# Kernel tuning notes

Measured on AMD Instinct MI355X. Metric: run time of the kernel, lower is better.

The kernel has to match this reference:

```python
import jax, jax.numpy as jnp
import numpy as np

B, L, H = 64, 512, 1024


def _gen_masks():
    rng = np.random.default_rng(0)

    def gen_cat(items_lo, items_hi, w_lo, w_hi, s_lo, s_hi):
        items_per_ex = rng.integers(items_lo, items_hi + 1, size=B)
        word_counts, sub_counts = [], []
        ex_sub = np.zeros(B, np.int64)
        ex_word = np.zeros(B, np.int64)
        for i in range(B):
            for _ in range(int(items_per_ex[i])):
                nw = int(rng.integers(w_lo, w_hi + 1))
                word_counts.append(nw)
                ex_word[i] += nw
                for _ in range(nw):
                    ns = int(rng.integers(s_lo, s_hi + 1))
                    sub_counts.append(ns)
                    ex_sub[i] += ns
        return items_per_ex, np.array(word_counts), np.array(sub_counts), ex_sub, ex_word

    q = gen_cat(1, 1, 8, 15, 1, 3)     # one question per example
    t = gen_cat(3, 6, 1, 3, 1, 3)      # tables per example
    c = gen_cat(12, 25, 1, 4, 1, 3)    # columns per example

    def plm_mask(starts, lens):
        m = np.zeros((B, L), bool)
        for i in range(B):
            m[i, starts[i]:starts[i] + lens[i]] = True
        return m

    qs = np.ones(B, np.int64)
    ts = qs + q[3]
    cs = ts + t[3]
    assert int((cs + c[3]).max()) <= L

    def sub_mask(sc):
        return np.arange(sc.max())[None, :] < sc[:, None]

    masks = dict(
        question_mask_plm=plm_mask(qs, q[3]),
        table_mask_plm=plm_mask(ts, t[3]),
        column_mask_plm=plm_mask(cs, c[3]),
        question_subword_mask=sub_mask(q[2]),
        table_subword_mask=sub_mask(t[2]),
        column_subword_mask=sub_mask(c[2]),
        question_mask=np.arange(q[4].max())[None, :] < q[4][:, None],
        table_word_mask=np.arange(t[1].max())[None, :] < t[1][:, None],
        column_word_mask=np.arange(c[1].max())[None, :] < c[1][:, None],
    )
    return {k: jnp.asarray(v) for k, v in masks.items()}


def setup_inputs() -> dict:
    key = jax.random.key(0)
    k1, k2 = jax.random.split(key)
    inp = _gen_masks()
    inp["inputs"] = jax.random.normal(k1, (B, L, H), jnp.float32)
    inp["W"] = jax.random.normal(k2, (H, H), jnp.float32) * 0.02
    inp["b"] = jnp.zeros((H,), jnp.float32)
    return inp


def _move(values, src_mask, dst_mask):
    """masked_select(src_mask) followed by masked_scatter_(dst_mask):
    the k-th True of src_mask feeds the k-th True of dst_mask (row-major)."""
    Hd = values.shape[-1]
    v = values.reshape(-1, Hd)
    sm = src_mask.reshape(-1)
    n = v.shape[0]
    rank = jnp.cumsum(sm) - 1                       # rank among True positions
    buf = jnp.zeros((n, Hd), v.dtype).at[jnp.where(sm, rank, n)].set(v, mode="drop")
    dm = dst_mask.reshape(-1)
    drank = jnp.clip(jnp.cumsum(dm) - 1, 0, n - 1)
    out = jnp.where(dm[:, None], buf[drank], 0.0)
    return out.reshape(dst_mask.shape + (Hd,))


def _scatter_rows(rows, dst_mask):
    """masked_scatter_ of consecutive row vectors into True slots of dst_mask."""
    dm = dst_mask.reshape(-1)
    rank = jnp.clip(jnp.cumsum(dm) - 1, 0, rows.shape[0] - 1)
    out = jnp.where(dm[:, None], rows[rank], 0.0)
    return out.reshape(dst_mask.shape + (rows.shape[-1],))


def _pool(x, mask, W, b):
    # PoolingFunction(method='mean-pooling'): masked mean over subwords, then Linear+Tanh
    mf = mask.astype(x.dtype)[..., None]
    mean = (x * mf).sum(1) / mf.sum(1)
    return jnp.tanh(mean @ W.T + b)


def _forward(inputs, W, b, m):
    q = _pool(_move(inputs, m["question_mask_plm"], m["question_subword_mask"]),
              m["question_subword_mask"], W, b)
    t = _pool(_move(inputs, m["table_mask_plm"], m["table_subword_mask"]),
              m["table_subword_mask"], W, b)
    c = _pool(_move(inputs, m["column_mask_plm"], m["column_subword_mask"]),
              m["column_subword_mask"], W, b)
    return (_scatter_rows(q, m["question_mask"]),
            _scatter_rows(t, m["table_word_mask"]),
            _scatter_rows(c, m["column_word_mask"]))


def reference(inputs, W, b, question_mask_plm, table_mask_plm, column_mask_plm,
              question_subword_mask, table_subword_mask, column_subword_mask,
              question_mask, table_word_mask, column_word_mask):
    m = dict(question_mask_plm=question_mask_plm, table_mask_plm=table_mask_plm,
             column_mask_plm=column_mask_plm, question_subword_mask=question_subword_mask,
             table_subword_mask=table_subword_mask, column_subword_mask=column_subword_mask,
             question_mask=question_mask, table_word_mask=table_word_mask,
             column_word_mask=column_word_mask)
    return _forward(inputs, W, b, m)
```

## Files before the change

### kernel.cpp

```cpp
#include <hip/hip_runtime.h>
#include <hip/hip_bf16.h>
#include <stdint.h>

#define BB 64
#define LL 512
#define HH 1024

using short8 = __attribute__((ext_vector_type(8))) short;
using f32x4  = __attribute__((ext_vector_type(4))) float;

static __device__ __forceinline__ unsigned short f2b(float x) {
    union { float f; uint32_t u; } t; t.f = x;
    uint32_t u = t.u;
    u += 0x7fffu + ((u >> 16) & 1u);
    return (unsigned short)(u >> 16);
}

__global__ __launch_bounds__(256)
void meta_kernel(const int* __restrict__ plm0, const int* __restrict__ plm1,
                 const int* __restrict__ plm2,
                 const int* __restrict__ sub0, const int* __restrict__ sub1,
                 const int* __restrict__ sub2,
                 const int* __restrict__ wm0, const int* __restrict__ wm1,
                 const int* __restrict__ wm2,
                 int ssub0, int ssub1, int ssub2,
                 int wmsz0, int wmsz1, int wmsz2,
                 int cap0, int cap1, int cap2,
                 int* __restrict__ g_src, int* __restrict__ g_ns,
                 int* __restrict__ g_orow)
{
    const int cat = blockIdx.x;
    const int* P    = (cat == 0) ? plm0 : (cat == 1) ? plm1 : plm2;
    const int* D    = (cat == 0) ? sub0 : (cat == 1) ? sub1 : sub2;
    const int* WM   = (cat == 0) ? wm0  : (cat == 1) ? wm1  : wm2;
    const int ssub  = (cat == 0) ? ssub0 : (cat == 1) ? ssub1 : ssub2;
    const int wmsz  = (cat == 0) ? wmsz0 : (cat == 1) ? wmsz1 : wmsz2;
    const int cap   = (cat == 0) ? cap0  : (cat == 1) ? cap1  : cap2;
    int wb = 0, rbase = 0;
    if (cat >= 1) { wb += cap0; rbase += wmsz0; }
    if (cat >= 2) { wb += cap1; rbase += wmsz1; }

    __shared__ int ex_f[BB];
    __shared__ int ex_sub_off[BB + 1];
    __shared__ int qf[256], qc[256];
    __shared__ int wsum[4];

    const int tid = threadIdx.x;
    const int lane = tid & 63;
    const int wv = tid >> 6;

    {
        const int row = tid & 63;
        const int quarter = tid >> 6;
        const int4* rp = reinterpret_cast<const int4*>(P + row * LL + quarter * 128);
        int c = 0, f = 0x7fffffff;
        #pragma unroll 8
        for (int i = 0; i < 32; ++i) {
            int4 v = rp[i];
            if (v.x) { ++c; if (f == 0x7fffffff) f = quarter * 128 + i * 4 + 0; }
            if (v.y) { ++c; if (f == 0x7fffffff) f = quarter * 128 + i * 4 + 1; }
            if (v.z) { ++c; if (f == 0x7fffffff) f = quarter * 128 + i * 4 + 2; }
            if (v.w) { ++c; if (f == 0x7fffffff) f = quarter * 128 + i * 4 + 3; }
        }
        qc[tid] = c;
        qf[tid] = f;
    }
    __syncthreads();
    if (tid < 64) {
        int c = qc[tid] + qc[tid + 64] + qc[tid + 128] + qc[tid + 192];
        int f = min(min(qf[tid], qf[tid + 64]), min(qf[tid + 128], qf[tid + 192]));
        ex_f[tid] = (f == 0x7fffffff) ? 0 : f;
        int v = c;
        #pragma unroll
        for (int off = 1; off < 64; off <<= 1) {
            int u = __shfl_up(v, off, 64);
            if (tid >= off) v += u;
        }
        ex_sub_off[tid + 1] = v;
        if (tid == 0) ex_sub_off[0] = 0;
    }
    __syncthreads();

    const int seg = (wmsz + 255) >> 8;
    const int p0 = tid * seg;
    const int p1 = min(p0 + seg, wmsz);
    int c = 0;
    for (int p = p0; p < p1; ++p) c += (WM[p] != 0);
    int incl = c;
    #pragma unroll
    for (int off = 1; off < 64; off <<= 1) {
        int u = __shfl_up(incl, off, 64);
        if (lane >= off) incl += u;
    }
    if (lane == 63) wsum[wv] = incl;
    __syncthreads();
    int woff = 0;
    for (int i = 0; i < wv; ++i) woff += wsum[i];
    const int NW = wsum[0] + wsum[1] + wsum[2] + wsum[3];
    int k = woff + incl - c;
    for (int p = p0; p < p1; ++p)
        if (WM[p]) g_orow[wb + (k++)] = rbase + p;

    for (int w = NW + tid; w < cap; w += 256) {
        g_orow[wb + w] = -1;
        g_ns[wb + w] = 0;
        g_src[wb + w] = 0;
    }

    const int Smax = (NW > 0) ? (ssub / NW) : 1;

    const int seg2 = (NW + 255) >> 8;
    const int w0 = tid * seg2;
    const int w1 = min(w0 + seg2, NW);
    int cs = 0;
    for (int w = w0; w < w1; ++w) {
        const int* dr = D + (size_t)w * Smax;
        for (int j = 0; j < Smax; ++j) cs += (dr[j] != 0);
    }
    __syncthreads();
    int incl2 = cs;
    #pragma unroll
    for (int off = 1; off < 64; off <<= 1) {
        int u = __shfl_up(incl2, off, 64);
        if (lane >= off) incl2 += u;
    }
    if (lane == 63) wsum[wv] = incl2;
    __syncthreads();
    int soff = 0;
    for (int i = 0; i < wv; ++i) soff += wsum[i];
    int subrank = soff + incl2 - cs;
    for (int w = w0; w < w1; ++w) {
        int ns = 0;
        const int* dr = D + (size_t)w * Smax;
        for (int j = 0; j < Smax; ++j) ns += (dr[j] != 0);
        int lo = 0, hi = BB;
        while (hi - lo > 1) {
            int mid = (lo + hi) >> 1;
            if (ex_sub_off[mid] <= subrank) lo = mid; else hi = mid;
        }
        g_src[wb + w] = lo * LL + ex_f[lo] + (subrank - ex_sub_off[lo]);
        g_ns[wb + w] = ns;
        subrank += ns;
    }
}

__global__ __launch_bounds__(256)
void means_kernel(const float* __restrict__ X, const int* __restrict__ g_src,
                  const int* __restrict__ g_ns, const int* __restrict__ g_orow,
                  unsigned short* __restrict__ meansB)
{
    const int w = blockIdx.x;
    if (g_orow[w] < 0) return;
    const int ns = g_ns[w];
    const int base = g_src[w];
    const int c0 = threadIdx.x * 4;
    float ax = 0.f, ay = 0.f, az = 0.f, aw = 0.f;
    for (int j = 0; j < ns; ++j) {
        const float4 v = *reinterpret_cast<const float4*>(
            X + (size_t)(base + j) * HH + c0);
        ax += v.x; ay += v.y; az += v.z; aw += v.w;
    }
    const float s = 1.0f / (float)ns;
    ushort4 o;
    o.x = f2b(ax * s); o.y = f2b(ay * s); o.z = f2b(az * s); o.w = f2b(aw * s);
    *reinterpret_cast<ushort4*>(meansB + (size_t)w * HH + c0) = o;
}

__global__ __launch_bounds__(256)
void wconv_kernel(const float* __restrict__ Wf, unsigned short* __restrict__ Wb)
{
    const int idx = (blockIdx.x * 256 + threadIdx.x) * 4;
    const float4 v = *reinterpret_cast<const float4*>(Wf + idx);
    ushort4 o;
    o.x = f2b(v.x); o.y = f2b(v.y); o.z = f2b(v.z); o.w = f2b(v.w);
    *reinterpret_cast<ushort4*>(Wb + idx) = o;
}

__global__ __launch_bounds__(256)
void gemm_kernel(const unsigned short* __restrict__ A,
                 const unsigned short* __restrict__ Wb,
                 const float* __restrict__ bias,
                 const int* __restrict__ g_orow,
                 float* __restrict__ out, int M_total)
{
    __shared__ unsigned short lb[64 * 72];

    const int m_base = blockIdx.x * 64;
    const int n_base = blockIdx.y * 64;
    const int tid = threadIdx.x;
    const int wv = tid >> 6;
    const int lane = tid & 63;
    const int q = lane >> 4;
    const int ml = lane & 15;

    const int row16 = m_base + wv * 16 + ml;
    const int orow_ml = (row16 < M_total) ? g_orow[row16] : -1;
    if (!__syncthreads_or(orow_ml >= 0)) return;

    f32x4 acc[4];
    #pragma unroll
    for (int t = 0; t < 4; ++t) acc[t] = (f32x4){0.f, 0.f, 0.f, 0.f};

    const int srow = tid >> 2;
    const int schunk = tid & 3;
    const unsigned short* Bsrc = Wb + (size_t)(n_base + srow) * HH + schunk * 16;
    unsigned short* Bdst = lb + srow * 72 + schunk * 16;

    const unsigned short* Ap = A + (size_t)row16 * HH + q * 8;
    const unsigned short* l0 = lb + ml * 72 + q * 8;

    for (int k0 = 0; k0 < HH; k0 += 64) {
        __syncthreads();
        *reinterpret_cast<short8*>(Bdst) =
            *reinterpret_cast<const short8*>(Bsrc + k0);
        *reinterpret_cast<short8*>(Bdst + 8) =
            *reinterpret_cast<const short8*>(Bsrc + k0 + 8);
        __syncthreads();
        const short8 a0 = *reinterpret_cast<const short8*>(Ap + k0);
        const short8 a1 = *reinterpret_cast<const short8*>(Ap + k0 + 32);
        #pragma unroll
        for (int nq = 0; nq < 4; ++nq) {
            const short8 b0 = *reinterpret_cast<const short8*>(l0 + nq * 16 * 72);
            acc[nq] = __builtin_amdgcn_mfma_f32_16x16x32_bf16(a0, b0, acc[nq], 0, 0, 0);
        }
        #pragma unroll
        for (int nq = 0; nq < 4; ++nq) {
            const short8 b1 = *reinterpret_cast<const short8*>(l0 + nq * 16 * 72 + 32);
            acc[nq] = __builtin_amdgcn_mfma_f32_16x16x32_bf16(a1, b1, acc[nq], 0, 0, 0);
        }
    }

    #pragma unroll
    for (int t = 0; t < 4; ++t) {
        const int col = n_base + t * 16 + ml;
        const float bv = bias[col];
        #pragma unroll
        for (int r = 0; r < 4; ++r) {
            const int row = m_base + wv * 16 + q * 4 + r;
            if (row < M_total) {
                const int orow = g_orow[row];
                if (orow >= 0) {
                    out[(size_t)orow * HH + col] = tanhf(acc[t][r] + bv);
                }
            }
        }
    }
}

extern "C" void kernel_launch(void* const* d_in, const int* in_sizes, int n_in,
                              void* d_out, int out_size, void* d_ws, size_t ws_size,
                              hipStream_t stream)
{
    const int* plm0 = (const int*)d_in[0];
    const int* plm1 = (const int*)d_in[1];
    const int* plm2 = (const int*)d_in[2];
    const int* sub0 = (const int*)d_in[3];
    const int* sub1 = (const int*)d_in[4];
    const int* sub2 = (const int*)d_in[5];
    const int* wm0  = (const int*)d_in[6];
    const int* wm1  = (const int*)d_in[7];
    const int* wm2  = (const int*)d_in[8];
    const float* X    = (const float*)d_in[9];
    const float* Wf   = (const float*)d_in[10];
    const float* bias = (const float*)d_in[11];

    const int wmsz0 = in_sizes[6], wmsz1 = in_sizes[7], wmsz2 = in_sizes[8];
    const int cap0 = (wmsz0 + 63) & ~63;
    const int cap1 = (wmsz1 + 63) & ~63;
    const int cap2 = (wmsz2 + 63) & ~63;
    const int Mslots = cap0 + cap1 + cap2;
    const int gx = Mslots / 64;

    char* ws = (char*)d_ws;
    unsigned short* Wb = (unsigned short*)ws;
    unsigned short* meansB = (unsigned short*)(ws + (size_t)HH * HH * 2);
    char* p = ws + (size_t)HH * HH * 2 + (size_t)Mslots * HH * 2;
    int* g_src  = (int*)p; p += (size_t)Mslots * 4;
    int* g_ns   = (int*)p; p += (size_t)Mslots * 4;
    int* g_orow = (int*)p;

    hipMemsetAsync(d_out, 0, (size_t)out_size * sizeof(float), stream);

    wconv_kernel<<<(HH * HH / 4) / 256, 256, 0, stream>>>(Wf, Wb);

    meta_kernel<<<3, 256, 0, stream>>>(plm0, plm1, plm2, sub0, sub1, sub2,
                                       wm0, wm1, wm2,
                                       in_sizes[3], in_sizes[4], in_sizes[5],
                                       wmsz0, wmsz1, wmsz2,
                                       cap0, cap1, cap2,
                                       g_src, g_ns, g_orow);

    means_kernel<<<Mslots, 256, 0, stream>>>(X, g_src, g_ns, g_orow, meansB);

    gemm_kernel<<<dim3(gx, 16), 256, 0, stream>>>(meansB, Wb, bias, g_orow,
                                                  (float*)d_out, Mslots);
}
```

Measured before the change: 281.2 us.

## Fuse W conversion into meta kernel, drop memset, gather GEMM rows by output index

Moves the fp32-to-bf16 weight conversion into extra blocks of the meta kernel and removes the full output memset. The GEMM now iterates over output rows and gathers A rows through an inverse map, writing zeros for padded rows itself and filling tiles that have no valid rows. The means kernel packs four words per block, one wave each. This cuts two launches and a full-output memset pass, at the cost of a more complex row-mapping scheme.

```diff
diff --git a/kernel.cpp b/kernel.cpp
--- a/kernel.cpp
+++ b/kernel.cpp
@@ -26,9 +26,21 @@
                  int ssub0, int ssub1, int ssub2,
                  int wmsz0, int wmsz1, int wmsz2,
                  int cap0, int cap1, int cap2,
+                 const float* __restrict__ Wf, unsigned short* __restrict__ Wb,
                  int* __restrict__ g_src, int* __restrict__ g_ns,
-                 int* __restrict__ g_orow)
+                 int* __restrict__ g_wrow)
 {
+    const int tid = threadIdx.x;
+
+    if (blockIdx.x >= 3) {
+        const int idx = ((blockIdx.x - 3) * 256 + tid) * 4;
+        const float4 v = *reinterpret_cast<const float4*>(Wf + idx);
+        ushort4 o;
+        o.x = f2b(v.x); o.y = f2b(v.y); o.z = f2b(v.z); o.w = f2b(v.w);
+        *reinterpret_cast<ushort4*>(Wb + idx) = o;
+        return;
+    }
+
     const int cat = blockIdx.x;
     const int* P    = (cat == 0) ? plm0 : (cat == 1) ? plm1 : plm2;
     const int* D    = (cat == 0) ? sub0 : (cat == 1) ? sub1 : sub2;
@@ -45,7 +57,6 @@
     __shared__ int qf[256], qc[256];
     __shared__ int wsum[4];
 
-    const int tid = threadIdx.x;
     const int lane = tid & 63;
     const int wv = tid >> 6;
 
@@ -79,6 +90,8 @@
         ex_sub_off[tid + 1] = v;
         if (tid == 0) ex_sub_off[0] = 0;
     }
+
+    for (int p = tid; p < wmsz; p += 256) g_wrow[rbase + p] = -1;
     __syncthreads();
 
     const int seg = (wmsz + 255) >> 8;
@@ -99,10 +112,9 @@
     const int NW = wsum[0] + wsum[1] + wsum[2] + wsum[3];
     int k = woff + incl - c;
     for (int p = p0; p < p1; ++p)
-        if (WM[p]) g_orow[wb + (k++)] = rbase + p;
+        if (WM[p]) g_wrow[rbase + p] = wb + (k++);
 
     for (int w = NW + tid; w < cap; w += 256) {
-        g_orow[wb + w] = -1;
         g_ns[wb + w] = 0;
         g_src[wb + w] = 0;
     }
@@ -146,42 +158,41 @@
 
 __global__ __launch_bounds__(256)
 void means_kernel(const float* __restrict__ X, const int* __restrict__ g_src,
-                  const int* __restrict__ g_ns, const int* __restrict__ g_orow,
+                  const int* __restrict__ g_ns,
                   unsigned short* __restrict__ meansB)
 {
-    const int w = blockIdx.x;
-    if (g_orow[w] < 0) return;
+    const int w = blockIdx.x * 4 + (threadIdx.x >> 6);
+    const int lane = threadIdx.x & 63;
     const int ns = g_ns[w];
+    if (ns == 0) return;
     const int base = g_src[w];
-    const int c0 = threadIdx.x * 4;
-    float ax = 0.f, ay = 0.f, az = 0.f, aw = 0.f;
+    float4 acc[4] = {{0,0,0,0},{0,0,0,0},{0,0,0,0},{0,0,0,0}};
     for (int j = 0; j < ns; ++j) {
-        const float4 v = *reinterpret_cast<const float4*>(
-            X + (size_t)(base + j) * HH + c0);
-        ax += v.x; ay += v.y; az += v.z; aw += v.w;
+        const float4* xp = reinterpret_cast<const float4*>(
+            X + (size_t)(base + j) * HH) + lane;
+        #pragma unroll
+        for (int ch = 0; ch < 4; ++ch) {
+            const float4 v = xp[ch * 64];
+            acc[ch].x += v.x; acc[ch].y += v.y; acc[ch].z += v.z; acc[ch].w += v.w;
+        }
     }
     const float s = 1.0f / (float)ns;
-    ushort4 o;
-    o.x = f2b(ax * s); o.y = f2b(ay * s); o.z = f2b(az * s); o.w = f2b(aw * s);
-    *reinterpret_cast<ushort4*>(meansB + (size_t)w * HH + c0) = o;
-}
-
-__global__ __launch_bounds__(256)
-void wconv_kernel(const float* __restrict__ Wf, unsigned short* __restrict__ Wb)
-{
-    const int idx = (blockIdx.x * 256 + threadIdx.x) * 4;
-    const float4 v = *reinterpret_cast<const float4*>(Wf + idx);
-    ushort4 o;
-    o.x = f2b(v.x); o.y = f2b(v.y); o.z = f2b(v.z); o.w = f2b(v.w);
-    *reinterpret_cast<ushort4*>(Wb + idx) = o;
+    ushort4* mp = reinterpret_cast<ushort4*>(meansB + (size_t)w * HH) + lane;
+    #pragma unroll
+    for (int ch = 0; ch < 4; ++ch) {
+        ushort4 o;
+        o.x = f2b(acc[ch].x * s); o.y = f2b(acc[ch].y * s);
+        o.z = f2b(acc[ch].z * s); o.w = f2b(acc[ch].w * s);
+        mp[ch * 64] = o;
+    }
 }
 
 __global__ __launch_bounds__(256)
 void gemm_kernel(const unsigned short* __restrict__ A,
                  const unsigned short* __restrict__ Wb,
                  const float* __restrict__ bias,
-                 const int* __restrict__ g_orow,
-                 float* __restrict__ out, int M_total)
+                 const int* __restrict__ g_wrow,
+                 float* __restrict__ out, int rows_total)
 {
     __shared__ unsigned short lb[64 * 72];
 
@@ -194,19 +205,29 @@
     const int ml = lane & 15;
 
     const int row16 = m_base + wv * 16 + ml;
-    const int orow_ml = (row16 < M_total) ? g_orow[row16] : -1;
-    if (!__syncthreads_or(orow_ml >= 0)) return;
+    int arow = (row16 < rows_total) ? g_wrow[row16] : -1;
+    if (!__syncthreads_or(arow >= 0)) {
+        const int zr = m_base + (tid >> 2);
+        if (zr < rows_total) {
+            float4 z = {0.f, 0.f, 0.f, 0.f};
+            float4* o = reinterpret_cast<float4*>(
+                out + (size_t)zr * HH + n_base + (tid & 3) * 16);
+            o[0] = z; o[1] = z; o[2] = z; o[3] = z;
+        }
+        return;
+    }
+    if (arow < 0) arow = 0;
 
     f32x4 acc[4];
     #pragma unroll
     for (int t = 0; t < 4; ++t) acc[t] = (f32x4){0.f, 0.f, 0.f, 0.f};
 
-    const int srow = tid >> 2;
+    const int srow_st = tid >> 2;
     const int schunk = tid & 3;
-    const unsigned short* Bsrc = Wb + (size_t)(n_base + srow) * HH + schunk * 16;
-    unsigned short* Bdst = lb + srow * 72 + schunk * 16;
-
-    const unsigned short* Ap = A + (size_t)row16 * HH + q * 8;
+    const unsigned short* Bsrc = Wb + (size_t)(n_base + srow_st) * HH + schunk * 16;
+    unsigned short* Bdst = lb + srow_st * 72 + schunk * 16;
+
+    const unsigned short* Ap = A + (size_t)arow * HH + q * 8;
     const unsigned short* l0 = lb + ml * 72 + q * 8;
 
     for (int k0 = 0; k0 < HH; k0 += 64) {
@@ -230,18 +251,19 @@
         }
     }
 
-    #pragma unroll
-    for (int t = 0; t < 4; ++t) {
-        const int col = n_base + t * 16 + ml;
-        const float bv = bias[col];
-        #pragma unroll
-        for (int r = 0; r < 4; ++r) {
-            const int row = m_base + wv * 16 + q * 4 + r;
-            if (row < M_total) {
-                const int orow = g_orow[row];
-                if (orow >= 0) {
-                    out[(size_t)orow * HH + col] = tanhf(acc[t][r] + bv);
-                }
+    float bv[4];
+    #pragma unroll
+    for (int t = 0; t < 4; ++t) bv[t] = bias[n_base + t * 16 + ml];
+    #pragma unroll
+    for (int r = 0; r < 4; ++r) {
+        const int srow = m_base + wv * 16 + q * 4 + r;
+        if (srow < rows_total) {
+            const int wr = g_wrow[srow];
+            #pragma unroll
+            for (int t = 0; t < 4; ++t) {
+                const int col = n_base + t * 16 + ml;
+                out[(size_t)srow * HH + col] =
+                    (wr >= 0) ? tanhf(acc[t][r] + bv[t]) : 0.0f;
             }
         }
     }
@@ -269,7 +291,8 @@
     const int cap1 = (wmsz1 + 63) & ~63;
     const int cap2 = (wmsz2 + 63) & ~63;
     const int Mslots = cap0 + cap1 + cap2;
-    const int gx = Mslots / 64;
+    const int rows_total = wmsz0 + wmsz1 + wmsz2;
+    const int gx = (rows_total + 63) / 64;
 
     char* ws = (char*)d_ws;
     unsigned short* Wb = (unsigned short*)ws;
@@ -277,21 +300,16 @@
     char* p = ws + (size_t)HH * HH * 2 + (size_t)Mslots * HH * 2;
     int* g_src  = (int*)p; p += (size_t)Mslots * 4;
     int* g_ns   = (int*)p; p += (size_t)Mslots * 4;
-    int* g_orow = (int*)p;
-
-    hipMemsetAsync(d_out, 0, (size_t)out_size * sizeof(float), stream);
-
-    wconv_kernel<<<(HH * HH / 4) / 256, 256, 0, stream>>>(Wf, Wb);
-
-    meta_kernel<<<3, 256, 0, stream>>>(plm0, plm1, plm2, sub0, sub1, sub2,
-                                       wm0, wm1, wm2,
-                                       in_sizes[3], in_sizes[4], in_sizes[5],
-                                       wmsz0, wmsz1, wmsz2,
-                                       cap0, cap1, cap2,
-                                       g_src, g_ns, g_orow);
-
-    means_kernel<<<Mslots, 256, 0, stream>>>(X, g_src, g_ns, g_orow, meansB);
-
-    gemm_kernel<<<dim3(gx, 16), 256, 0, stream>>>(meansB, Wb, bias, g_orow,
-                                                  (float*)d_out, Mslots);
-}
+    int* g_wrow = (int*)p;
+
+    meta_kernel<<<3 + (HH * HH / 4) / 256, 256, 0, stream>>>(
+        plm0, plm1, plm2, sub0, sub1, sub2, wm0, wm1, wm2,
+        in_sizes[3], in_sizes[4], in_sizes[5],
+        wmsz0, wmsz1, wmsz2, cap0, cap1, cap2,
+        Wf, Wb, g_src, g_ns, g_wrow);
+
+    means_kernel<<<Mslots / 4, 256, 0, stream>>>(X, g_src, g_ns, meansB);
+
+    gemm_kernel<<<dim3(gx, 16), 256, 0, stream>>>(meansB, Wb, bias, g_wrow,
+                                                  (float*)d_out, rows_total);
+}
```

Measured after the change: 276.1 us. No clear change (-1.8%).
